# Kernel optimization log

Measured on AMD Instinct MI355X. Metric: run time of the kernel, lower is better.

Reference implementation:

```python
import jax, jax.numpy as jnp
import numpy as np

N_NODES = 100000
N_EDGES = 3200000
D_IN, D_HID, D_OUT = 128, 128, 40


def _sage_conv(x, src, dst, W_l, W_r, b, counts):
    # mean aggregation of neighbor (source) features at destination nodes
    agg = jax.ops.segment_sum(x[src], dst, num_segments=N_NODES)  # [N, d]
    agg = agg / counts  # mean (isolated nodes stay zero via clamped counts)
    # PyG SAGEConv: out = lin_l(aggr) + lin_r(x_root); bias lives in lin_l
    return agg @ W_l + x @ W_r + b


def setup_inputs() -> dict:
    key = jax.random.key(0)
    ks = jax.random.split(key, 8)
    x = jax.random.normal(ks[0], (N_NODES, D_IN), dtype=jnp.float32)
    edge_index = jax.random.randint(ks[1], (2, N_EDGES), 0, N_NODES, dtype=jnp.int64)
    s1 = 1.0 / np.sqrt(D_IN)
    s2 = 1.0 / np.sqrt(D_HID)
    return {
        "x": x,
        "edge_index": edge_index,
        "W1_l": jax.random.uniform(ks[2], (D_IN, D_HID), jnp.float32, -s1, s1),
        "W1_r": jax.random.uniform(ks[3], (D_IN, D_HID), jnp.float32, -s1, s1),
        "b1": jnp.zeros((D_HID,), jnp.float32),
        "W2_l": jax.random.uniform(ks[4], (D_HID, D_OUT), jnp.float32, -s2, s2),
        "W2_r": jax.random.uniform(ks[5], (D_HID, D_OUT), jnp.float32, -s2, s2),
        "b2": jnp.zeros((D_OUT,), jnp.float32),
    }


def reference(x, edge_index, W1_l, W1_r, b1, W2_l, W2_r, b2):
    src, dst = edge_index[0], edge_index[1]
    # in-degree per destination node, clamped to avoid div-by-zero
    deg = jax.ops.segment_sum(jnp.ones((N_EDGES,), jnp.float32), dst, num_segments=N_NODES)
    counts = jnp.maximum(deg, 1.0)[:, None]  # [N, 1]
    h = jax.nn.relu(_sage_conv(x, src, dst, W1_l, W1_r, b1, counts))
    h = _sage_conv(h, src, dst, W2_l, W2_r, b2, counts)
    return jax.nn.log_softmax(h, axis=1)
```

## Files before the change

### kernel.cpp

```cpp
#include <hip/hip_runtime.h>
#include <hip/hip_bf16.h>
#include <hip/hip_fp8.h>
#include <math.h>

#define N_NODES 100000
#define D_IN    128
#define D_HID   128
#define D_OUT   40
#define NBUCK   391
#define CHUNK   8192
#define SLABCAP 16320
#define CAST_BLOCKS_1K 1563


using short8  = __attribute__((ext_vector_type(8))) short;
using float4v = __attribute__((ext_vector_type(4))) float;
using floatx2 = __attribute__((ext_vector_type(2))) float;

__device__ __forceinline__ unsigned short f2b(float f) {
    __hip_bfloat16 b = __float2bfloat16(f);
    return *(unsigned short*)&b;
}
__device__ __forceinline__ unsigned packb(float a, float b) {
    return (unsigned)f2b(a) | ((unsigned)f2b(b) << 16);
}

__device__ __forceinline__ unsigned char f2q(float f) {
    __hip_fp8_e4m3 v(f);
    return *(unsigned char*)&v;
}
template <int SEL>
__device__ __forceinline__ float q2f(unsigned u) {
#if __has_builtin(__builtin_amdgcn_cvt_f32_fp8)
    return __builtin_amdgcn_cvt_f32_fp8((int)u, SEL);
#else
    unsigned char b = (u >> (SEL * 8)) & 0xff;
    __hip_fp8_e4m3 v;
    *(unsigned char*)&v = b;
    return (float)v;
#endif
}
template <bool HI>
__device__ __forceinline__ floatx2 pkcvt(unsigned u) {
#if __has_builtin(__builtin_amdgcn_cvt_pk_f32_fp8)
    return __builtin_amdgcn_cvt_pk_f32_fp8((int)u, HI);
#else
    floatx2 r;
    if constexpr (HI) { r[0] = q2f<2>(u); r[1] = q2f<3>(u); }
    else              { r[0] = q2f<0>(u); r[1] = q2f<1>(u); }
    return r;
#endif
}

__device__ __forceinline__ long long edge_at(const void* ei, int is64, long long idx) {
    if (is64) return ((const long long*)ei)[idx];
    return (long long)((const int*)ei)[idx];
}

__global__ __launch_bounds__(256) void init_kernel(const int* __restrict__ ei,
                                                   int* __restrict__ flag,
                                                   unsigned* __restrict__ bcount) {
    const int t = threadIdx.x;
    if (t < 64) {
        int ok = 1;
#pragma unroll
        for (int k = 0; k < 4; ++k) {
            if (ei[2 * (t * 4 + k) + 1] != 0) ok = 0;
        }
        int all0 = __all(ok);
        if (t == 0) *flag = all0 ? 1 : 0;
    }
    if (t < NBUCK) bcount[t] = 0u;
    if (t + 256 < NBUCK) bcount[t + 256] = 0u;
}

__global__ __launch_bounds__(1024) void mega_kernel(const void* __restrict__ ei,
                                                    const int* __restrict__ flag,
                                                    unsigned* __restrict__ bcount,
                                                    unsigned* __restrict__ slab,
                                                    long long E, int npb,
                                                    const float* __restrict__ x,
                                                    unsigned short* __restrict__ xb,
                                                    unsigned char* __restrict__ xq,
                                                    const float* __restrict__ W1l,
                                                    const float* __restrict__ W1r,
                                                    const float* __restrict__ W2l,
                                                    const float* __restrict__ W2r,
                                                    unsigned short* __restrict__ wp1,
                                                    unsigned short* __restrict__ wp2) {
    __shared__ unsigned hist[NBUCK];
    __shared__ unsigned lstart[NBUCK];
    __shared__ unsigned gofs[NBUCK];
    __shared__ unsigned s[512];
    __shared__ unsigned wsum[16];
    __shared__ unsigned rec[CHUNK];
    __shared__ unsigned short bkt[CHUNK];

    const int blk = blockIdx.x;
    const int tid = threadIdx.x;

    if (blk >= npb) {
        const int cb = blk - npb;
        if (cb < CAST_BLOCKS_1K) {
            long long i = ((long long)cb * 1024 + tid) * 8;
            if (i >= (long long)N_NODES * 128) return;
            float4 a = *(const float4*)&x[i];
            float4 c = *(const float4*)&x[i + 4];
            ushort4 o0, o1;
            o0.x = f2b(a.x); o0.y = f2b(a.y); o0.z = f2b(a.z); o0.w = f2b(a.w);
            o1.x = f2b(c.x); o1.y = f2b(c.y); o1.z = f2b(c.z); o1.w = f2b(c.w);
            *(ushort4*)&xb[i] = o0;
            *(ushort4*)&xb[i + 4] = o1;
            uint2 p;
            p.x = (unsigned)f2q(a.x) | ((unsigned)f2q(a.y) << 8)
                | ((unsigned)f2q(a.z) << 16) | ((unsigned)f2q(a.w) << 24);
            p.y = (unsigned)f2q(c.x) | ((unsigned)f2q(c.y) << 8)
                | ((unsigned)f2q(c.z) << 16) | ((unsigned)f2q(c.w) << 24);
            *(uint2*)&xq[i] = p;
        } else {
            int t = (cb - CAST_BLOCKS_1K) * 1024 + tid;
            if (t < 4096) {
                int lane = t & 63;
                int ks = (t >> 6) & 7;
                int ct = t >> 9;
                int n = ct * 16 + (lane & 15);
                int kr = (lane >> 4) * 8;
                unsigned short v[8];
#pragma unroll
                for (int j = 0; j < 8; ++j) {
                    int k = ks * 32 + kr + j;
                    float f = (k < 128) ? W1l[k * 128 + n] : W1r[(k - 128) * 128 + n];
                    v[j] = f2b(f);
                }
                ushort4 o0 = {v[0], v[1], v[2], v[3]};
                ushort4 o1 = {v[4], v[5], v[6], v[7]};
                *(ushort4*)&wp1[t * 8] = o0;
                *(ushort4*)&wp1[t * 8 + 4] = o1;
            } else if (t < 4096 + 1280) {
                int u = t - 4096;
                int lane = u & 63;
                int ks = (u >> 6) & 3;
                int ct = u >> 8;
                int n = ct * 16 + (lane & 15);
                int kr = (lane >> 4) * 8;
                unsigned short v[8];
#pragma unroll
                for (int j = 0; j < 8; ++j) {
                    int k = ks * 32 + kr + j;
                    float f = (n < 40) ? W2l[k * 40 + n] : W2r[k * 40 + (n - 40)];
                    v[j] = f2b(f);
                }
                ushort4 o0 = {v[0], v[1], v[2], v[3]};
                ushort4 o1 = {v[4], v[5], v[6], v[7]};
                *(ushort4*)&wp2[u * 8] = o0;
                *(ushort4*)&wp2[u * 8 + 4] = o1;
            }
        }
        return;
    }

    const int lane = tid & 63;
    const int w = tid >> 6;
    const int is64 = *flag;
    const long long cb64 = (long long)blk * CHUNK;
    const unsigned n = (unsigned)(((E - cb64) < (long long)CHUNK) ? (E - cb64) : CHUNK);

    if (tid < NBUCK) hist[tid] = 0;
    __syncthreads();

    unsigned esrc[CHUNK / 1024], edst[CHUNK / 1024];
#pragma unroll
    for (int j = 0; j < CHUNK / 1024; ++j) {
        unsigned e = j * 1024 + tid;
        if (e < n) {
            esrc[j] = (unsigned)edge_at(ei, is64, cb64 + e);
            edst[j] = (unsigned)edge_at(ei, is64, E + cb64 + e);
            atomicAdd(&hist[edst[j] >> 8], 1u);
        }
    }
    __syncthreads();

    {
        unsigned v0 = (tid < NBUCK) ? hist[tid] : 0u;
        unsigned xx = v0;
#pragma unroll
        for (int off = 1; off < 64; off <<= 1) {
            unsigned t = __shfl_up(xx, off);
            if (lane >= off) xx += t;
        }
        if (lane == 63) wsum[w] = xx;
        __syncthreads();
        if (w == 0) {
            unsigned y = (lane < 16) ? wsum[lane] : 0u;
#pragma unroll
            for (int off = 1; off < 16; off <<= 1) {
                unsigned t = __shfl_up(y, off);
                if (lane >= off) y += t;
            }
            if (lane < 16) wsum[lane] = y;
        }
        __syncthreads();
        unsigned pre = (w > 0) ? wsum[w - 1] : 0u;
        if (tid < NBUCK) s[tid] = xx + pre;
    }
    if (tid < NBUCK) {
        unsigned cnt = hist[tid];
        unsigned ex = s[tid] - cnt;
        lstart[tid] = ex;
        if (cnt) {
            unsigned g = atomicAdd(&bcount[tid], cnt);
            gofs[tid] = (unsigned)(tid * SLABCAP) + g - ex;
        }
        hist[tid] = 0;
    }
    __syncthreads();

#pragma unroll
    for (int j = 0; j < CHUNK / 1024; ++j) {
        unsigned e = j * 1024 + tid;
        if (e < n) {
            unsigned d = edst[j];
            unsigned b = d >> 8;
            unsigned loc = atomicAdd(&hist[b], 1u);
            unsigned slot = lstart[b] + loc;
            rec[slot] = ((d & 255u) << 17) | esrc[j];
            bkt[slot] = (unsigned short)b;
        }
    }
    __syncthreads();

#pragma unroll
    for (int j = 0; j < CHUNK / 1024; ++j) {
        unsigned i = j * 1024 + tid;
        if (i < n) {
            unsigned b = bkt[i];
            slab[gofs[b] + i] = rec[i];
        }
    }
}

__global__ __launch_bounds__(256) void build_kernel(const unsigned* __restrict__ slab,
                                                    const unsigned* __restrict__ bcount,
                                                    unsigned* __restrict__ deg,
                                                    float* __restrict__ invc,
                                                    unsigned* __restrict__ row_start,
                                                    int* __restrict__ csr) {
    __shared__ unsigned red[4];
    __shared__ unsigned ws[4];
    __shared__ unsigned cnt[256];
    const int tid = threadIdx.x;
    const int lane = tid & 63;
    const int w = tid >> 6;
    const int nb = blockIdx.x << 8;
    const long long sb = (long long)blockIdx.x * SLABCAP;

    unsigned pv = 0;
    for (unsigned i = tid; i < (unsigned)blockIdx.x; i += 256) pv += bcount[i];
#pragma unroll
    for (int off = 32; off >= 1; off >>= 1) pv += __shfl_xor(pv, off);
    if (lane == 0) red[w] = pv;
    __syncthreads();
    const unsigned es = red[0] + red[1] + red[2] + red[3];
    const unsigned n  = bcount[blockIdx.x];

    cnt[tid] = 0;
    __syncthreads();
    for (unsigned i = tid; i < n; i += 256) {
        unsigned d = slab[sb + i] >> 17;
        atomicAdd(&cnt[d], 1u);
    }
    __syncthreads();
    unsigned v = cnt[tid];
    unsigned x = v;
#pragma unroll
    for (int off = 1; off < 64; off <<= 1) {
        unsigned t = __shfl_up(x, off);
        if (lane >= off) x += t;
    }
    if (lane == 63) ws[w] = x;
    __syncthreads();
    unsigned pre = 0;
#pragma unroll
    for (int k = 0; k < 4; ++k) if (k < w) pre += ws[k];
    unsigned ex = x + pre - v;
    int node = nb + tid;
    if (node < N_NODES) {
        deg[node] = v;
        invc[node] = 1.0f / fmaxf((float)v, 1.0f);
        row_start[node] = es + ex;
    }
    __syncthreads();
    cnt[tid] = ex;
    __syncthreads();
    for (unsigned i = tid; i < n; i += 256) {
        unsigned pr = slab[sb + i];
        unsigned d = pr >> 17;
        unsigned pos = es + atomicAdd(&cnt[d], 1u);
        csr[pos] = (int)(pr & 0x1FFFFu);
    }
}

__global__ __launch_bounds__(256) void gather_fp8_kernel(const unsigned char* __restrict__ featq,
                                                         const int* __restrict__ csr,
                                                         const unsigned* __restrict__ row_start,
                                                         const unsigned* __restrict__ deg,
                                                         const float* __restrict__ invc,
                                                         unsigned short* __restrict__ aggb) {
    const int wave = threadIdx.x >> 6;
    const int lane = threadIdx.x & 63;
    const int node = blockIdx.x * 4 + wave;
    if (node >= N_NODES) return;

    const unsigned start = row_start[node];
    const unsigned cnt = deg[node];
    const int s = lane >> 4;
    const unsigned cgo = (unsigned)((lane & 15) * 8);

    floatx2 acc[4];
#pragma unroll
    for (int k = 0; k < 4; ++k) acc[k] = (floatx2){0.f, 0.f};

    for (unsigned base = 0; base < cnt; base += 64) {
        unsigned rem = cnt - base;
        if (rem > 64u) rem = 64u;
        int nid = (lane < (int)rem) ? csr[start + base + lane] : 0;
        for (unsigned j = 0; j < rem; j += 8) {
            uint2 u0 = {0u, 0u}, u1 = {0u, 0u};
            unsigned i0 = j + s;
            unsigned i1 = j + 4 + s;
            int s0 = __shfl(nid, (int)(i0 & 63));
            int s1 = __shfl(nid, (int)(i1 & 63));
            if (i0 < rem) u0 = *(const uint2*)&featq[((unsigned)s0 << 7) + cgo];
            if (i1 < rem) u1 = *(const uint2*)&featq[((unsigned)s1 << 7) + cgo];
            acc[0] += pkcvt<false>(u0.x); acc[1] += pkcvt<true>(u0.x);
            acc[2] += pkcvt<false>(u0.y); acc[3] += pkcvt<true>(u0.y);
            acc[0] += pkcvt<false>(u1.x); acc[1] += pkcvt<true>(u1.x);
            acc[2] += pkcvt<false>(u1.y); acc[3] += pkcvt<true>(u1.y);
        }
    }

#pragma unroll
    for (int k = 0; k < 4; ++k) {
        acc[k][0] += __shfl_xor(acc[k][0], 16);
        acc[k][1] += __shfl_xor(acc[k][1], 16);
        acc[k][0] += __shfl_xor(acc[k][0], 32);
        acc[k][1] += __shfl_xor(acc[k][1], 32);
    }

    if (lane < 16) {
        const float ic = invc[node];
        uint4 o;
        o.x = packb(acc[0][0] * ic, acc[0][1] * ic);
        o.y = packb(acc[1][0] * ic, acc[1][1] * ic);
        o.z = packb(acc[2][0] * ic, acc[2][1] * ic);
        o.w = packb(acc[3][0] * ic, acc[3][1] * ic);
        *(uint4*)&aggb[(unsigned)node * 128u + cgo] = o;
    }
}

__global__ __launch_bounds__(256) void gemm12_kernel(const unsigned short* __restrict__ aggb,
                                                     const unsigned short* __restrict__ xb,
                                                     const unsigned short* __restrict__ wp1,
                                                     const float* __restrict__ b1,
                                                     const unsigned short* __restrict__ wp2,
                                                     const float* __restrict__ b2,
                                                     unsigned char* __restrict__ pq,
                                                     float* __restrict__ q) {
    __shared__ unsigned short sh[64][136];
    const int wave = threadIdx.x >> 6;
    const int lane = threadIdx.x & 63;
    const int row0 = blockIdx.x * 64 + wave * 16;
    const unsigned abase = (unsigned)(row0 + (lane & 15)) * 128u + (unsigned)((lane >> 4) * 8);

    float4v acc[8];
#pragma unroll
    for (int ct = 0; ct < 8; ++ct) acc[ct] = (float4v){0.f, 0.f, 0.f, 0.f};

#pragma unroll
    for (int ks = 0; ks < 8; ++ks) {
        union { uint4 u; short8 s; } af;
        if (ks < 4) af.u = *(const uint4*)&aggb[abase + ks * 32];
        else        af.u = *(const uint4*)&xb[abase + (ks - 4) * 32];
#pragma unroll
        for (int ct = 0; ct < 8; ++ct) {
            union { uint4 u; short8 s; } bf;
            bf.u = *(const uint4*)&wp1[((ct * 8 + ks) * 64 + lane) * 8];
            acc[ct] = __builtin_amdgcn_mfma_f32_16x16x32_bf16(af.s, bf.s, acc[ct], 0, 0, 0);
        }
    }

    const int lrow0 = wave * 16 + (lane >> 4) * 4;
    const int ccol = lane & 15;
#pragma unroll
    for (int ct = 0; ct < 8; ++ct) {
        const int col = ct * 16 + ccol;
        const float bv = b1[col];
#pragma unroll
        for (int r = 0; r < 4; ++r)
            sh[lrow0 + r][col] = f2b(fmaxf(acc[ct][r] + bv, 0.0f));
    }

    const unsigned short* aptr = &sh[wave * 16 + (lane & 15)][(lane >> 4) * 8];

    float4v acc2[5];
#pragma unroll
    for (int ct = 0; ct < 5; ++ct) acc2[ct] = (float4v){0.f, 0.f, 0.f, 0.f};

#pragma unroll
    for (int ks = 0; ks < 4; ++ks) {
        union { uint4 u; short8 s; } af;
        af.u = *(const uint4*)&aptr[ks * 32];
#pragma unroll
        for (int ct = 0; ct < 5; ++ct) {
            union { uint4 u; short8 s; } bf;
            bf.u = *(const uint4*)&wp2[((ct * 4 + ks) * 64 + lane) * 8];
            acc2[ct] = __builtin_amdgcn_mfma_f32_16x16x32_bf16(af.s, bf.s, acc2[ct], 0, 0, 0);
        }
    }

    const int crow0 = row0 + (lane >> 4) * 4;
#pragma unroll
    for (int ct = 0; ct < 5; ++ct) {
        const int col = ct * 16 + ccol;
#pragma unroll
        for (int r = 0; r < 4; ++r) {
            int row = crow0 + r;
            if (row < N_NODES) {
                if (col < D_OUT) {
                    pq[(unsigned)row * 40u + (unsigned)col] = f2q(acc2[ct][r]);
                } else {
                    q[(unsigned)row * 40u + (unsigned)(col - D_OUT)] = acc2[ct][r] + b2[col - D_OUT];
                }
            }
        }
    }
}

__global__ __launch_bounds__(256) void gather40_kernel(const unsigned char* __restrict__ pq,
                                                       const float* __restrict__ q,
                                                       const int* __restrict__ csr,
                                                       const unsigned* __restrict__ row_start,
                                                       const unsigned* __restrict__ deg,
                                                       const float* __restrict__ invc,
                                                       float* __restrict__ out) {
    __shared__ float sm[4][40];
    const int wave = threadIdx.x >> 6;
    const int lane = threadIdx.x & 63;
    const int node = blockIdx.x * 4 + wave;
    if (node >= N_NODES) return;

    const unsigned start = row_start[node];
    const unsigned cnt = deg[node];
    const int s = lane / 10;
    const int cg = lane % 10;
    const unsigned cgo = (unsigned)(cg * 4);
    const bool gactive = s < 6;

    floatx2 a01 = (floatx2){0.f, 0.f}, a23 = (floatx2){0.f, 0.f};

    for (unsigned base = 0; base < cnt; base += 64) {
        unsigned rem = cnt - base;
        if (rem > 64u) rem = 64u;
        int nid = (lane < (int)rem) ? csr[start + base + lane] : 0;
        for (unsigned j = 0; j < rem; j += 24) {
            unsigned u[4];
#pragma unroll
            for (int t = 0; t < 4; ++t) {
                unsigned idx = j + t * 6 + s;
                int sid = __shfl(nid, (int)(idx & 63));
                bool valid = gactive && (idx < rem);
                u[t] = valid ? *(const unsigned*)&pq[(unsigned)sid * 40u + cgo] : 0u;
            }
#pragma unroll
            for (int t = 0; t < 4; ++t) {
                a01 += pkcvt<false>(u[t]);
                a23 += pkcvt<true>(u[t]);
            }
        }
    }

    float a0 = a01[0], a1 = a01[1], a2 = a23[0], a3 = a23[1];
    {
        float t0, t1, t2, t3;
        t0 = __shfl(a0, lane + 30); t1 = __shfl(a1, lane + 30);
        t2 = __shfl(a2, lane + 30); t3 = __shfl(a3, lane + 30);
        if (lane < 30) { a0 += t0; a1 += t1; a2 += t2; a3 += t3; }
        t0 = __shfl(a0, lane + 20); t1 = __shfl(a1, lane + 20);
        t2 = __shfl(a2, lane + 20); t3 = __shfl(a3, lane + 20);
        if (lane < 10) { a0 += t0; a1 += t1; a2 += t2; a3 += t3; }
        t0 = __shfl(a0, lane + 10); t1 = __shfl(a1, lane + 10);
        t2 = __shfl(a2, lane + 10); t3 = __shfl(a3, lane + 10);
        if (lane < 10) { a0 += t0; a1 += t1; a2 += t2; a3 += t3; }
    }
    if (lane < 10) {
        sm[wave][cg * 4 + 0] = a0;
        sm[wave][cg * 4 + 1] = a1;
        sm[wave][cg * 4 + 2] = a2;
        sm[wave][cg * 4 + 3] = a3;
    }
    const bool active = lane < D_OUT;
    float v = active ? (sm[wave][active ? lane : 0] * invc[node]
                        + q[(unsigned)node * 40u + (unsigned)(active ? lane : 0)])
                     : -__builtin_huge_valf();
    float m = v;
#pragma unroll
    for (int off = 32; off >= 1; off >>= 1) m = fmaxf(m, __shfl_xor(m, off));
    float e = active ? expf(v - m) : 0.0f;
    float ssum = e;
#pragma unroll
    for (int off = 32; off >= 1; off >>= 1) ssum += __shfl_xor(ssum, off);
    float ls = logf(ssum);
    if (active) out[(unsigned)node * 40u + (unsigned)lane] = v - m - ls;
}

extern "C" void kernel_launch(void* const* d_in, const int* in_sizes, int n_in,
                              void* d_out, int out_size, void* d_ws, size_t ws_size,
                              hipStream_t stream) {
    const float* x   = (const float*)d_in[0];
    const void*  ei  = d_in[1];
    const float* W1l = (const float*)d_in[2];
    const float* W1r = (const float*)d_in[3];
    const float* b1  = (const float*)d_in[4];
    const float* W2l = (const float*)d_in[5];
    const float* W2r = (const float*)d_in[6];
    const float* b2  = (const float*)d_in[7];
    float* out = (float*)d_out;

    const long long E = (long long)in_sizes[1] / 2;
    const int NPB = (int)((E + CHUNK - 1) / CHUNK);

    char* ws = (char*)d_ws;
    int*      flag      = (int*)ws;
    unsigned* bcount    = (unsigned*)(ws + 4096);
    unsigned* deg       = (unsigned*)(ws + 16384);
    float*    invc      = (float*)(ws + 416384);
    unsigned* row_start = (unsigned*)(ws + 816384);
    int*      csr       = (int*)(ws + 1216384);
    unsigned short* xb  = (unsigned short*)(ws + 14016384);
    unsigned short* aggb= (unsigned short*)(ws + 39616384);
    unsigned* slab      = (unsigned*)(ws + 39616384);
    unsigned short* wp1 = (unsigned short*)(ws + 65216384);
    unsigned short* wp2 = (unsigned short*)(ws + 65281920);
    unsigned char*  pq  = (unsigned char*)(ws + 65310720);
    float*    q         = (float*)(ws + 69310720);
    unsigned char*  xq  = (unsigned char*)(ws + 90910720);

    init_kernel<<<1, 256, 0, stream>>>((const int*)ei, flag, bcount);

    mega_kernel<<<NPB + CAST_BLOCKS_1K + 6, 1024, 0, stream>>>(
        ei, flag, bcount, slab, E, NPB,
        x, xb, xq, W1l, W1r, W2l, W2r, wp1, wp2);

    build_kernel<<<NBUCK, 256, 0, stream>>>(slab, bcount, deg, invc, row_start, csr);

    gather_fp8_kernel<<<(N_NODES + 3) / 4, 256, 0, stream>>>(xq, csr, row_start, deg, invc, aggb);
    gemm12_kernel<<<(N_NODES + 63) / 64, 256, 0, stream>>>(aggb, xb, wp1, b1, wp2, b2, pq, q);

    gather40_kernel<<<(N_NODES + 3) / 4, 256, 0, stream>>>(pq, q, csr, row_start, deg, invc, out);
}
```

Baseline: 301.7 us.

## Replace global bucket atomics with per-chunk offset table and drop init kernel

The edge-bucketing pass no longer reserves global slab space with atomicAdd on per-bucket counters. Each chunk block now writes its locally sorted records to a contiguous per-chunk slab region and publishes its per-bucket exclusive offsets into a table. The build kernel rebuilds each bucket by prefix-summing those offsets across chunks and copying the runs into a shared-memory stage before counting and scattering. The separate init kernel is removed, with the int64/int32 index detection moved inline into each block. This removes one launch, the global atomics and the bucket-id scratch, but the build kernel now does serial, scattered run copies that may be latency bound.

Result: no change. 297.0 us, median of 2 (-1.6%).

```diff
diff --git a/kernel.cpp b/kernel.cpp
--- a/kernel.cpp
+++ b/kernel.cpp
@@ -9,7 +9,7 @@
 #define D_OUT   40
 #define NBUCK   391
 #define CHUNK   8192
-#define SLABCAP 16320
+#define STAGECAP 12160
 #define CAST_BLOCKS_1K 1563
 
 
@@ -57,27 +57,9 @@
     return (long long)((const int*)ei)[idx];
 }
 
-__global__ __launch_bounds__(256) void init_kernel(const int* __restrict__ ei,
-                                                   int* __restrict__ flag,
-                                                   unsigned* __restrict__ bcount) {
-    const int t = threadIdx.x;
-    if (t < 64) {
-        int ok = 1;
-#pragma unroll
-        for (int k = 0; k < 4; ++k) {
-            if (ei[2 * (t * 4 + k) + 1] != 0) ok = 0;
-        }
-        int all0 = __all(ok);
-        if (t == 0) *flag = all0 ? 1 : 0;
-    }
-    if (t < NBUCK) bcount[t] = 0u;
-    if (t + 256 < NBUCK) bcount[t + 256] = 0u;
-}
-
 __global__ __launch_bounds__(1024) void mega_kernel(const void* __restrict__ ei,
-                                                    const int* __restrict__ flag,
-                                                    unsigned* __restrict__ bcount,
                                                     unsigned* __restrict__ slab,
+                                                    unsigned* __restrict__ lofs,
                                                     long long E, int npb,
                                                     const float* __restrict__ x,
                                                     unsigned short* __restrict__ xb,
@@ -90,11 +72,9 @@
                                                     unsigned short* __restrict__ wp2) {
     __shared__ unsigned hist[NBUCK];
     __shared__ unsigned lstart[NBUCK];
-    __shared__ unsigned gofs[NBUCK];
-    __shared__ unsigned s[512];
     __shared__ unsigned wsum[16];
     __shared__ unsigned rec[CHUNK];
-    __shared__ unsigned short bkt[CHUNK];
+    __shared__ int sflag[1];
 
     const int blk = blockIdx.x;
     const int tid = threadIdx.x;
@@ -161,12 +141,23 @@
 
     const int lane = tid & 63;
     const int w = tid >> 6;
-    const int is64 = *flag;
+
+    if (w == 0) {
+        const int* e32 = (const int*)ei;
+        int ok = 1;
+#pragma unroll
+        for (int k = 0; k < 4; ++k) {
+            if (e32[2 * (lane * 4 + k) + 1] != 0) ok = 0;
+        }
+        int all0 = __all(ok);
+        if (lane == 0) sflag[0] = all0;
+    }
+    if (tid < NBUCK) hist[tid] = 0;
+    __syncthreads();
+    const int is64 = sflag[0];
+
     const long long cb64 = (long long)blk * CHUNK;
     const unsigned n = (unsigned)(((E - cb64) < (long long)CHUNK) ? (E - cb64) : CHUNK);
-
-    if (tid < NBUCK) hist[tid] = 0;
-    __syncthreads();
 
     unsigned esrc[CHUNK / 1024], edst[CHUNK / 1024];
 #pragma unroll
@@ -201,17 +192,13 @@
         }
         __syncthreads();
         unsigned pre = (w > 0) ? wsum[w - 1] : 0u;
-        if (tid < NBUCK) s[tid] = xx + pre;
-    }
-    if (tid < NBUCK) {
-        unsigned cnt = hist[tid];
-        unsigned ex = s[tid] - cnt;
-        lstart[tid] = ex;
-        if (cnt) {
-            unsigned g = atomicAdd(&bcount[tid], cnt);
-            gofs[tid] = (unsigned)(tid * SLABCAP) + g - ex;
-        }
-        hist[tid] = 0;
+        if (tid < NBUCK) {
+            unsigned ex = xx + pre - v0;
+            lstart[tid] = ex;
+            lofs[(unsigned)tid * (unsigned)npb + (unsigned)blk] = ex;
+            hist[tid] = 0;
+        }
+        if (tid == 0) lofs[(unsigned)NBUCK * (unsigned)npb + (unsigned)blk] = n;
     }
     __syncthreads();
 
@@ -222,9 +209,7 @@
             unsigned d = edst[j];
             unsigned b = d >> 8;
             unsigned loc = atomicAdd(&hist[b], 1u);
-            unsigned slot = lstart[b] + loc;
-            rec[slot] = ((d & 255u) << 17) | esrc[j];
-            bkt[slot] = (unsigned short)b;
+            rec[lstart[b] + loc] = ((d & 255u) << 17) | esrc[j];
         }
     }
     __syncthreads();
@@ -232,42 +217,76 @@
 #pragma unroll
     for (int j = 0; j < CHUNK / 1024; ++j) {
         unsigned i = j * 1024 + tid;
-        if (i < n) {
-            unsigned b = bkt[i];
-            slab[gofs[b] + i] = rec[i];
-        }
+        if (i < n) slab[(unsigned)blk * (unsigned)CHUNK + i] = rec[i];
     }
 }
 
 __global__ __launch_bounds__(256) void build_kernel(const unsigned* __restrict__ slab,
-                                                    const unsigned* __restrict__ bcount,
+                                                    const unsigned* __restrict__ lofs,
+                                                    int npb,
                                                     unsigned* __restrict__ deg,
                                                     float* __restrict__ invc,
                                                     unsigned* __restrict__ row_start,
                                                     int* __restrict__ csr) {
-    __shared__ unsigned red[4];
-    __shared__ unsigned ws[4];
+    __shared__ unsigned rstart[NBUCK];
+    __shared__ unsigned rcnt[NBUCK];
+    __shared__ unsigned pofs[NBUCK];
+    __shared__ unsigned redlds[4];
+    __shared__ unsigned wsum2[4];
     __shared__ unsigned cnt[256];
+    __shared__ unsigned stage[STAGECAP];
+
     const int tid = threadIdx.x;
     const int lane = tid & 63;
     const int w = tid >> 6;
-    const int nb = blockIdx.x << 8;
-    const long long sb = (long long)blockIdx.x * SLABCAP;
-
-    unsigned pv = 0;
-    for (unsigned i = tid; i < (unsigned)blockIdx.x; i += 256) pv += bcount[i];
-#pragma unroll
-    for (int off = 32; off >= 1; off >>= 1) pv += __shfl_xor(pv, off);
-    if (lane == 0) red[w] = pv;
-    __syncthreads();
-    const unsigned es = red[0] + red[1] + red[2] + red[3];
-    const unsigned n  = bcount[blockIdx.x];
+    const int b = blockIdx.x;
+    const int nb = b << 8;
+
+    unsigned psum = 0;
+    for (int p = tid; p < npb; p += 256) {
+        unsigned lo = lofs[(unsigned)b * (unsigned)npb + (unsigned)p];
+        unsigned hi = lofs[(unsigned)(b + 1) * (unsigned)npb + (unsigned)p];
+        rstart[p] = lo;
+        rcnt[p] = hi - lo;
+        psum += lo;
+    }
+#pragma unroll
+    for (int off = 32; off >= 1; off >>= 1) psum += __shfl_xor(psum, off);
+    if (lane == 0) redlds[w] = psum;
+    __syncthreads();
+    const unsigned es = redlds[0] + redlds[1] + redlds[2] + redlds[3];
+
+    if (w == 0) {
+        unsigned carry = 0;
+        for (int r = 0; r < (npb + 63) / 64; ++r) {
+            int p = r * 64 + lane;
+            unsigned c = (p < npb) ? rcnt[p] : 0u;
+            unsigned x = c;
+#pragma unroll
+            for (int off = 1; off < 64; off <<= 1) {
+                unsigned t = __shfl_up(x, off);
+                if (lane >= off) x += t;
+            }
+            if (p < npb) pofs[p] = x - c + carry;
+            carry += __shfl(x, 63);
+        }
+    }
+    __syncthreads();
+    const unsigned n = pofs[npb - 1] + rcnt[npb - 1];
+
+    for (int p = tid; p < npb; p += 256) {
+        unsigned src = (unsigned)p * (unsigned)CHUNK + rstart[p];
+        unsigned dst = pofs[p];
+        unsigned c = rcnt[p];
+        for (unsigned i = 0; i < c; ++i)
+            stage[dst + i] = slab[src + i];
+    }
+    __syncthreads();
 
     cnt[tid] = 0;
     __syncthreads();
     for (unsigned i = tid; i < n; i += 256) {
-        unsigned d = slab[sb + i] >> 17;
-        atomicAdd(&cnt[d], 1u);
+        atomicAdd(&cnt[stage[i] >> 17], 1u);
     }
     __syncthreads();
     unsigned v = cnt[tid];
@@ -277,11 +296,11 @@
         unsigned t = __shfl_up(x, off);
         if (lane >= off) x += t;
     }
-    if (lane == 63) ws[w] = x;
+    if (lane == 63) wsum2[w] = x;
     __syncthreads();
     unsigned pre = 0;
 #pragma unroll
-    for (int k = 0; k < 4; ++k) if (k < w) pre += ws[k];
+    for (int k = 0; k < 4; ++k) if (k < w) pre += wsum2[k];
     unsigned ex = x + pre - v;
     int node = nb + tid;
     if (node < N_NODES) {
@@ -293,7 +312,7 @@
     cnt[tid] = ex;
     __syncthreads();
     for (unsigned i = tid; i < n; i += 256) {
-        unsigned pr = slab[sb + i];
+        unsigned pr = stage[i];
         unsigned d = pr >> 17;
         unsigned pos = es + atomicAdd(&cnt[d], 1u);
         csr[pos] = (int)(pr & 0x1FFFFu);
@@ -530,8 +549,6 @@
     const int NPB = (int)((E + CHUNK - 1) / CHUNK);
 
     char* ws = (char*)d_ws;
-    int*      flag      = (int*)ws;
-    unsigned* bcount    = (unsigned*)(ws + 4096);
     unsigned* deg       = (unsigned*)(ws + 16384);
     float*    invc      = (float*)(ws + 416384);
     unsigned* row_start = (unsigned*)(ws + 816384);
@@ -544,14 +561,13 @@
     unsigned char*  pq  = (unsigned char*)(ws + 65310720);
     float*    q         = (float*)(ws + 69310720);
     unsigned char*  xq  = (unsigned char*)(ws + 90910720);
-
-    init_kernel<<<1, 256, 0, stream>>>((const int*)ei, flag, bcount);
+    unsigned* lofs      = (unsigned*)(ws + 103710720);
 
     mega_kernel<<<NPB + CAST_BLOCKS_1K + 6, 1024, 0, stream>>>(
-        ei, flag, bcount, slab, E, NPB,
+        ei, slab, lofs, E, NPB,
         x, xb, xq, W1l, W1r, W2l, W2r, wp1, wp2);
 
-    build_kernel<<<NBUCK, 256, 0, stream>>>(slab, bcount, deg, invc, row_start, csr);
+    build_kernel<<<NBUCK, 256, 0, stream>>>(slab, lofs, NPB, deg, invc, row_start, csr);
 
     gather_fp8_kernel<<<(N_NODES + 3) / 4, 256, 0, stream>>>(xq, csr, row_start, deg, invc, aggb);
     gemm12_kernel<<<(N_NODES + 63) / 64, 256, 0, stream>>>(aggb, xb, wp1, b1, wp2, b2, pq, q);
```
